# Optimization experiments

Measured on AMD Instinct MI355X. Metric: run time of the kernel, lower is better.

## Reference

```python
import math
import jax, jax.numpy as jnp
import numpy as np

B, N, C = 2, 2048, 4096
NUM_HEADS, KV_HEADS, HEAD_DIM = 32, 8, 128
N_REP = NUM_HEADS // KV_HEADS  # num_key_value_groups
MAX_SEQ = 4096


def rotate_half(x):
    h = x.shape[-1] // 2
    return jnp.concatenate([-x[..., h:], x[..., :h]], axis=-1)


def setup_inputs() -> dict:
    key = jax.random.key(0)
    k1, k2 = jax.random.split(key)
    inp = jax.random.normal(k1, (B, N, C), jnp.float32)
    sz = NUM_HEADS * HEAD_DIM + 2 * KV_HEADS * HEAD_DIM  # 6144
    weight = jax.random.normal(k2, (sz, C), jnp.float32) * 0.02
    # real LLaMA rotary caches [1,1,MAX_SEQ,HEAD_DIM]
    inv_freq = 1.0 / (10000.0 ** (jnp.arange(0, HEAD_DIM, 2, dtype=jnp.float32) / HEAD_DIM))
    t = jnp.arange(MAX_SEQ, dtype=jnp.float32)
    freqs = jnp.outer(t, inv_freq)
    emb = jnp.concatenate([freqs, freqs], axis=-1)
    cos_cached = jnp.cos(emb)[None, None]
    sin_cached = jnp.sin(emb)[None, None]
    neg = jnp.finfo(jnp.float32).min
    causal = jnp.where(jnp.tril(jnp.ones((N, N), dtype=bool)), 0.0, neg)
    attention_mask = jnp.broadcast_to(causal[None, None], (B, 1, N, N))
    position_ids = jnp.broadcast_to(jnp.arange(N, dtype=jnp.int32), (B, N))
    observation_mask = jnp.ones((B, N), dtype=jnp.int32)
    return dict(input=inp, weight=weight, cos_cached=cos_cached, sin_cached=sin_cached,
                attention_mask=attention_mask, position_ids=position_ids,
                observation_mask=observation_mask)


def reference(input, weight, cos_cached, sin_cached, attention_mask, position_ids, observation_mask):
    b, n, c = input.shape
    dtype = input.dtype
    qkv = input @ weight.T  # [B,N,6144]
    sz_q = NUM_HEADS * HEAD_DIM
    sz_kv = KV_HEADS * HEAD_DIM
    q = qkv[:, :, :sz_q].reshape(b, n, NUM_HEADS, HEAD_DIM).transpose(0, 2, 1, 3)
    k = qkv[:, :, sz_q:sz_q + sz_kv].reshape(b, n, KV_HEADS, HEAD_DIM).transpose(0, 2, 1, 3)
    v = qkv[:, :, sz_q + sz_kv:].reshape(b, n, KV_HEADS, HEAD_DIM).transpose(0, 2, 1, 3)
    # inline RoPE (HF llama apply_rotary_pos_emb)
    cos = cos_cached[0, 0][position_ids][:, None]  # [B,1,N,D]
    sin = sin_cached[0, 0][position_ids][:, None]
    q = q * cos + rotate_half(q) * sin
    k = k * cos + rotate_half(k) * sin
    # repeat_kv: expand kv heads to match q heads (each kv head repeated contiguously)
    k = jnp.repeat(k, N_REP, axis=1)
    v = jnp.repeat(v, N_REP, axis=1)
    attn = jnp.einsum('bhqd,bhkd->bhqk', q / math.sqrt(HEAD_DIM), k)
    attn = attn + attention_mask
    attn = jnp.maximum(attn, jnp.finfo(dtype).min)
    attn = jax.nn.softmax(attn.astype(jnp.float32), axis=-1).astype(dtype)
    out = jnp.einsum('bhqk,bhkd->bqhd', attn, v).reshape(b, n, c)
    # output[observation_mask == 1]: with an all-ones mask this is the flat [B*N, C] output;
    # expressed jit-safely as a multiplicative select
    out = out.reshape(b * n, c) * (observation_mask.reshape(-1, 1) == 1)
    return out.astype(jnp.float32)
```

## Files before the change

kernel.cpp:

```cpp
#include <hip/hip_runtime.h>
#include <hip/hip_bf16.h>
#include <stdint.h>

typedef __attribute__((ext_vector_type(8))) short bf16x8;
typedef __attribute__((ext_vector_type(4))) float f32x4;
typedef __attribute__((ext_vector_type(16))) float f32x16;

#define NB 2
#define NSEQ 2048
#define CDIM 4096
#define NH 32
#define NKV 8
#define HD 128
#define QKV_COLS 6144

static __device__ __forceinline__ unsigned short f2bf(float f) {
    union { float f; unsigned int u; } v; v.f = f;
    unsigned int r = v.u + 0x7fff + ((v.u >> 16) & 1);
    return (unsigned short)(r >> 16);
}
static __device__ __forceinline__ float bf2f(unsigned short b) {
    union { unsigned int u; float f; } v; v.u = ((unsigned int)b) << 16;
    return v.f;
}

static __device__ __forceinline__ void glds16(const void* g, void* l) {
    __builtin_amdgcn_global_load_lds(
        (const __attribute__((address_space(1))) void*)g,
        (__attribute__((address_space(3))) void*)l, 16, 0, 0);
}

static __device__ __forceinline__ unsigned cvtpk(float a, float b) {
    unsigned r; asm("v_cvt_pk_bf16_f32 %0, %1, %2" : "=v"(r) : "v"(a), "v"(b));
    return r;
}

static __device__ __forceinline__ void pack_tile(const f32x16& p, int l, bf16x8& fa, bf16x8& fb) {
    unsigned a0 = cvtpk(p[0], p[1]),   b0 = cvtpk(p[4], p[5]);
    unsigned a1 = cvtpk(p[2], p[3]),   b1 = cvtpk(p[6], p[7]);
    unsigned a2 = cvtpk(p[8], p[9]),   b2 = cvtpk(p[12], p[13]);
    unsigned a3 = cvtpk(p[10], p[11]), b3 = cvtpk(p[14], p[15]);
    union U { unsigned u[4]; bf16x8 v; } ua, ub;
#if __has_builtin(__builtin_amdgcn_permlane32_swap)
    auto r0 = __builtin_amdgcn_permlane32_swap(a0, b0, false, false);
    auto r1 = __builtin_amdgcn_permlane32_swap(a1, b1, false, false);
    auto r2 = __builtin_amdgcn_permlane32_swap(a2, b2, false, false);
    auto r3 = __builtin_amdgcn_permlane32_swap(a3, b3, false, false);
    ua.u[0] = r0[0]; ua.u[1] = r1[0]; ua.u[2] = r0[1]; ua.u[3] = r1[1];
    ub.u[0] = r2[0]; ub.u[1] = r3[0]; ub.u[2] = r2[1]; ub.u[3] = r3[1];
#else
    unsigned a0t = __shfl_xor(a0, 32), b0t = __shfl_xor(b0, 32);
    unsigned a1t = __shfl_xor(a1, 32), b1t = __shfl_xor(b1, 32);
    unsigned a2t = __shfl_xor(a2, 32), b2t = __shfl_xor(b2, 32);
    unsigned a3t = __shfl_xor(a3, 32), b3t = __shfl_xor(b3, 32);
    bool lo = (l < 32);
    ua.u[0] = lo ? a0 : b0t; ua.u[1] = lo ? a1 : b1t; ua.u[2] = lo ? a0t : b0; ua.u[3] = lo ? a1t : b1;
    ub.u[0] = lo ? a2 : b2t; ub.u[1] = lo ? a3 : b3t; ub.u[2] = lo ? a2t : b2; ub.u[3] = lo ? a3t : b3;
#endif
    fa = ua.v; fb = ub.v;
}

__global__ void convert_kernel(const float* __restrict__ inA, const float* __restrict__ inW,
                               unsigned short* __restrict__ outA, unsigned short* __restrict__ outW) {
    const long long nA4 = (long long)CDIM * (NB * NSEQ) / 4;
    const long long nW4 = (long long)QKV_COLS * CDIM / 4;
    const long long total = nA4 + nW4;
    for (long long i = blockIdx.x * 256LL + threadIdx.x; i < total; i += (long long)gridDim.x * 256LL) {
        const float4* src; unsigned short* dst; long long j;
        if (i < nA4) { src = (const float4*)inA; dst = outA; j = i; }
        else         { src = (const float4*)inW; dst = outW; j = i - nA4; }
        float4 v = src[j];
        ushort4 o;
        o.x = f2bf(v.x); o.y = f2bf(v.y); o.z = f2bf(v.z); o.w = f2bf(v.w);
        ((ushort4*)dst)[j] = o;
    }
}

#define GPHASE(PP, VNSTR, STAGES) do {                                                        \
    const int r0_ = wm*128 + (PP*2)*16 + lr16;                                                \
    const int r1_ = r0_ + 16;                                                                 \
    bf16x8 a00 = *(const bf16x8*)(lds + cur*32768 + r0_*128 + ((lc4*16) ^ ((r0_&7)<<4)));     \
    bf16x8 a01 = *(const bf16x8*)(lds + cur*32768 + r0_*128 + ((64+lc4*16) ^ ((r0_&7)<<4)));  \
    bf16x8 a10 = *(const bf16x8*)(lds + cur*32768 + r1_*128 + ((lc4*16) ^ ((r1_&7)<<4)));     \
    bf16x8 a11 = *(const bf16x8*)(lds + cur*32768 + r1_*128 + ((64+lc4*16) ^ ((r1_&7)<<4)));  \
    if (PP == 0) {                                                                            \
        _Pragma("unroll")                                                                     \
        for (int nf = 0; nf < 3; ++nf) {                                                      \
            int rb = wn*48 + nf*16 + lr16;                                                    \
            bfr[nf][0] = *(const bf16x8*)(lds + 65536 + cur*24576 + rb*128 + ((lc4*16) ^ ((rb&7)<<4)));    \
            bfr[nf][1] = *(const bf16x8*)(lds + 65536 + cur*24576 + rb*128 + ((64+lc4*16) ^ ((rb&7)<<4))); \
        }                                                                                     \
    }                                                                                         \
    STAGES;                                                                                   \
    __builtin_amdgcn_s_barrier();                                                             \
    asm volatile("s_waitcnt lgkmcnt(0)" ::: "memory");                                        \
    __builtin_amdgcn_s_setprio(1);                                                            \
    _Pragma("unroll")                                                                         \
    for (int nf = 0; nf < 3; ++nf) {                                                          \
        acc[PP*2  ][nf] = __builtin_amdgcn_mfma_f32_16x16x32_bf16(a00, bfr[nf][0], acc[PP*2  ][nf], 0,0,0); \
        acc[PP*2  ][nf] = __builtin_amdgcn_mfma_f32_16x16x32_bf16(a01, bfr[nf][1], acc[PP*2  ][nf], 0,0,0); \
        acc[PP*2+1][nf] = __builtin_amdgcn_mfma_f32_16x16x32_bf16(a10, bfr[nf][0], acc[PP*2+1][nf], 0,0,0); \
        acc[PP*2+1][nf] = __builtin_amdgcn_mfma_f32_16x16x32_bf16(a11, bfr[nf][1], acc[PP*2+1][nf], 0,0,0); \
    }                                                                                         \
    __builtin_amdgcn_s_setprio(0);                                                            \
    asm volatile("s_waitcnt " VNSTR ::: "memory");                                            \
    __builtin_amdgcn_s_barrier();                                                             \
} while (0)

__global__ __launch_bounds__(512) void gemm_qkv8(
    const unsigned short* __restrict__ A, const unsigned short* __restrict__ W,
    unsigned short* __restrict__ qb, unsigned short* __restrict__ kb, unsigned short* __restrict__ vt)
{
    __shared__ unsigned char lds[114688];
    const int bid0 = blockIdx.x;
    const int swz = (bid0 & 7) * 64 + (bid0 >> 3);
    const int bm = swz >> 5, bn = swz & 31;
    const int tid = threadIdx.x, l = tid & 63, w = tid >> 6;
    const int wm = w >> 2, wn = w & 3;
    const int lr16 = l & 15, lc4 = l >> 4;
    const int tid16 = tid * 16;
    const int abase = (tid >> 8) * 16384 + (tid & 255) * 16;

    f32x4 acc[8][3] = {};
    bf16x8 bfr[3][2];

    auto stageA = [&](int tb, int kt, int d) {
        int r = d >> 7, c = d & 127;
        int cs = c ^ ((r & 7) << 4);
        glds16(A + (long long)(bm * 256 + r) * CDIM + kt * 64 + (cs >> 1), lds + tb * 32768 + d);
    };
    auto stageB = [&](int tb, int kt, int d) {
        int r = d >> 7, c = d & 127;
        int cs = c ^ ((r & 7) << 4);
        glds16(W + (long long)(bn * 192 + r) * CDIM + kt * 64 + (cs >> 1), lds + 65536 + tb * 24576 + d);
    };

    stageB(0, 0, tid16); stageB(0, 0, tid16 + 8192); stageB(0, 0, tid16 + 16384);
    stageA(0, 0, abase); stageA(0, 0, abase + 4096); stageA(0, 0, abase + 8192); stageA(0, 0, abase + 12288);
    asm volatile("s_waitcnt vmcnt(0)" ::: "memory");
    __builtin_amdgcn_s_barrier();

    for (int t = 0; t < 64; ++t) {
        const int cur = t & 1, tb = cur ^ 1;
        const int tn = (t + 1 < 64) ? t + 1 : 63;
        GPHASE(0, "vmcnt(4)", { stageB(tb, tn, tid16);         stageB(tb, tn, tid16 + 8192); });
        GPHASE(1, "vmcnt(5)", { stageB(tb, tn, tid16 + 16384); stageA(tb, tn, abase);        });
        GPHASE(2, "vmcnt(6)", { stageA(tb, tn, abase + 4096);  stageA(tb, tn, abase + 8192); });
        GPHASE(3, "vmcnt(3)", { stageA(tb, tn, abase + 12288); });
    }

#pragma unroll
    for (int mf = 0; mf < 8; ++mf) {
        int gm0 = bm * 256 + wm * 128 + mf * 16 + lc4 * 4;
        int b = gm0 >> 11, n0 = gm0 & 2047;
#pragma unroll
        for (int nf = 0; nf < 3; ++nf) {
            int coln = bn * 192 + wn * 48 + nf * 16 + lr16;
            if (coln < 4096) {
                unsigned short* dst = qb + (((long long)(b * NH + (coln >> 7)) * NSEQ + n0) << 7) + (coln & 127);
#pragma unroll
                for (int r = 0; r < 4; ++r) dst[(long long)r << 7] = f2bf(acc[mf][nf][r]);
            } else if (coln < 5120) {
                int ck = coln - 4096;
                unsigned short* dst = kb + (((long long)(b * NKV + (ck >> 7)) * NSEQ + n0) << 7) + (ck & 127);
#pragma unroll
                for (int r = 0; r < 4; ++r) dst[(long long)r << 7] = f2bf(acc[mf][nf][r]);
            } else {
                int cv = coln - 5120;
                ushort4 o4;
                o4.x = f2bf(acc[mf][nf][0]); o4.y = f2bf(acc[mf][nf][1]);
                o4.z = f2bf(acc[mf][nf][2]); o4.w = f2bf(acc[mf][nf][3]);
                *(ushort4*)(vt + (((long long)(b * NKV + (cv >> 7)) * HD + (cv & 127)) << 11) + n0) = o4;
            }
        }
    }
}

__global__ void rope_kernel(unsigned short* __restrict__ qb, unsigned short* __restrict__ kb,
                            const float* __restrict__ cosc, const float* __restrict__ sinc,
                            const int* __restrict__ pos) {
    int rowid = blockIdx.x * 4 + (threadIdx.x >> 6);
    int d = threadIdx.x & 63;
    int b = rowid / (40 * NSEQ);
    int rem = rowid % (40 * NSEQ);
    int head = rem / NSEQ, n = rem % NSEQ;
    unsigned short* p;
    float scale;
    if (head < NH) { p = qb + (((long long)(b * NH + head) * NSEQ + n) << 7); scale = 0.12751747934f; }
    else           { p = kb + (((long long)(b * NKV + (head - NH)) * NSEQ + n) << 7); scale = 1.0f; }
    int pid = pos[b * NSEQ + n];
    float c = cosc[pid * HD + d], s = sinc[pid * HD + d];
    float x0 = bf2f(p[d]), x1 = bf2f(p[d + 64]);
    p[d]      = f2bf((x0 * c - x1 * s) * scale);
    p[d + 64] = f2bf((x1 * c + x0 * s) * scale);
}

__global__ __launch_bounds__(512) void attn_kernel(
    const unsigned short* __restrict__ qb, const unsigned short* __restrict__ kb,
    const unsigned short* __restrict__ vt, const int* __restrict__ obs,
    float* __restrict__ out)
{
    __shared__ unsigned char k_tile[2][16384];
    __shared__ unsigned char v_tile[2][16384];

    const int bid = blockIdx.x;
    const int qt = 7 - (bid >> 6);
    const int bh = bid & 63;
    const int b = bh >> 5, h = bh & 31, kvh = h >> 2;
    const int t = threadIdx.x, l = t & 63, w = t >> 6;
    const int lr = l & 31, hi = l >> 5;
    const int swl = (l & 7) << 4;

    const unsigned short* Qb = qb + (((long long)(b * NH + h) * NSEQ + qt * 256 + w * 32) << 7);
    const unsigned short* Kb = kb + (((long long)(b * NKV + kvh) * NSEQ) << 7);
    const unsigned short* Vb = vt + (((long long)(b * NKV + kvh) * HD) << 11);

    bf16x8 qf[8];
#pragma unroll
    for (int dk = 0; dk < 8; ++dk)
        qf[dk] = *(const bf16x8*)(Qb + lr * 128 + dk * 16 + hi * 8);

    f32x16 o[4];
#pragma unroll
    for (int dt = 0; dt < 4; ++dt)
#pragma unroll
        for (int e = 0; e < 16; ++e) o[dt][e] = 0.f;
    float m_run = -1e30f, l_run = 0.f;

    const int qwmax = qt * 256 + w * 32 + 31;
    const int niter = 4 * qt + 4;

    auto stage = [&](int kt, int tb) {
#pragma unroll
        for (int i = 0; i < 2; ++i) {
            int byte = (i * 512 + t) * 16;
            { int r = byte >> 8, c = byte & 255; int cs = c ^ ((r & 7) << 4);
              glds16(Kb + (((long long)(kt * 64 + r)) << 7) + (cs >> 1), k_tile[tb] + byte); }
            { int r = byte >> 7, c = byte & 127; int cs = c ^ ((r & 7) << 4);
              glds16(Vb + (((long long)r) << 11) + kt * 64 + (cs >> 1), v_tile[tb] + byte); }
        }
    };

    stage(0, 0);
    asm volatile("s_waitcnt vmcnt(0)" ::: "memory");
    __syncthreads();

    for (int kt = 0; kt < niter; ++kt) {
        const int cur = kt & 1;
        if (kt + 1 < niter) stage(kt + 1, cur ^ 1);

        if (kt * 64 <= qwmax) {
            f32x16 s0, s1;
#pragma unroll
            for (int e = 0; e < 16; ++e) { s0[e] = 0.f; s1[e] = 0.f; }
            __builtin_amdgcn_s_setprio(1);
#pragma unroll
            for (int dk = 0; dk < 8; ++dk) {
                int cb = (dk * 32 + hi * 16) ^ swl;
                bf16x8 k0 = *(const bf16x8*)(k_tile[cur] + lr * 256 + cb);
                bf16x8 k1 = *(const bf16x8*)(k_tile[cur] + (32 + lr) * 256 + cb);
                s0 = __builtin_amdgcn_mfma_f32_32x32x16_bf16(k0, qf[dk], s0, 0, 0, 0);
                s1 = __builtin_amdgcn_mfma_f32_32x32x16_bf16(k1, qf[dk], s1, 0, 0, 0);
            }
            __builtin_amdgcn_s_setprio(0);

            if (kt * 64 + 63 > qt * 256 + w * 32) {
                int qg = qt * 256 + w * 32 + lr;
                int base = kt * 64 + hi * 4;
#pragma unroll
                for (int e = 0; e < 16; ++e) {
                    int kv0 = base + (e & 3) + 8 * (e >> 2);
                    if (kv0 > qg)      s0[e] = -1e30f;
                    if (kv0 + 32 > qg) s1[e] = -1e30f;
                }
            }

            float mloc = fmaxf(s0[0], s0[1]);
#pragma unroll
            for (int e = 2; e < 16; ++e) mloc = fmaxf(mloc, s0[e]);
#pragma unroll
            for (int e = 0; e < 16; ++e) mloc = fmaxf(mloc, s1[e]);
            mloc = fmaxf(mloc, __shfl_xor(mloc, 32));

            float mm = m_run;
            if (!__all(mloc - m_run <= 8.f)) {
                mm = fmaxf(m_run, mloc);
                float sc = __builtin_amdgcn_exp2f(m_run - mm);
                l_run *= sc;
#pragma unroll
                for (int dt = 0; dt < 4; ++dt)
#pragma unroll
                    for (int e = 0; e < 16; ++e) o[dt][e] *= sc;
                m_run = mm;
            }
            float sum = 0.f;
#pragma unroll
            for (int e = 0; e < 16; ++e) { s0[e] = __builtin_amdgcn_exp2f(s0[e] - mm); sum += s0[e]; }
#pragma unroll
            for (int e = 0; e < 16; ++e) { s1[e] = __builtin_amdgcn_exp2f(s1[e] - mm); sum += s1[e]; }
            sum += __shfl_xor(sum, 32);
            l_run += sum;

            bf16x8 pb[4];
            pack_tile(s0, l, pb[0], pb[1]);
            pack_tile(s1, l, pb[2], pb[3]);

            __builtin_amdgcn_s_setprio(1);
#pragma unroll
            for (int dt = 0; dt < 4; ++dt) {
#pragma unroll
                for (int kk = 0; kk < 4; ++kk) {
                    int cb = (kk * 32 + hi * 16) ^ swl;
                    bf16x8 vf = *(const bf16x8*)(v_tile[cur] + (dt * 32 + lr) * 128 + cb);
                    o[dt] = __builtin_amdgcn_mfma_f32_32x32x16_bf16(vf, pb[kk], o[dt], 0, 0, 0);
                }
            }
            __builtin_amdgcn_s_setprio(0);
        }

        asm volatile("s_waitcnt vmcnt(0)" ::: "memory");
        __syncthreads();
    }

    {
        int n = qt * 256 + w * 32 + lr;
        float fac = (1.f / l_run) * ((obs[b * NSEQ + n] == 1) ? 1.f : 0.f);
        unsigned char* slice = &k_tile[0][0] + w * 4096;
        int q2 = l >> 1, half = l & 1;
        long long orow = ((long long)(b * NSEQ + qt * 256 + w * 32 + q2)) << 12;
#pragma unroll
        for (int dt = 0; dt < 4; ++dt) {
#pragma unroll
            for (int e = 0; e < 16; e += 2) {
                int dl = (e & 3) + 8 * (e >> 2) + hi * 4;
                int byte = (lr * 128 + dl * 4) ^ ((lr & 7) << 4);
                *(float2*)(slice + byte) = make_float2(o[dt][e] * fac, o[dt][e + 1] * fac);
            }
#pragma unroll
            for (int j = 0; j < 4; ++j) {
                int byte = (q2 * 128 + half * 64 + j * 16) ^ ((q2 & 7) << 4);
                f32x4 vv = *(const f32x4*)(slice + byte);
                *(f32x4*)(out + orow + h * 128 + dt * 32 + half * 16 + j * 4) = vv;
            }
            __syncthreads();
        }
    }
}

extern "C" void kernel_launch(void* const* d_in, const int* in_sizes, int n_in,
                              void* d_out, int out_size, void* d_ws, size_t ws_size,
                              hipStream_t stream) {
    (void)in_sizes; (void)n_in; (void)out_size; (void)ws_size;
    const float* inp  = (const float*)d_in[0];
    const float* wgt  = (const float*)d_in[1];
    const float* cosc = (const float*)d_in[2];
    const float* sinc = (const float*)d_in[3];
    const int* pos = (const int*)d_in[5];
    const int* obs = (const int*)d_in[6];
    float* out = (float*)d_out;

    char* ws = (char*)d_ws;
    unsigned short* A16 = (unsigned short*)(ws);
    unsigned short* W16 = (unsigned short*)(ws + 33554432LL);
    unsigned short* qb  = (unsigned short*)(ws + 83886080LL);
    unsigned short* kb  = (unsigned short*)(ws + 117440512LL);
    unsigned short* vt  = (unsigned short*)(ws + 125829120LL);

    convert_kernel<<<2048, 256, 0, stream>>>(inp, wgt, A16, W16);
    gemm_qkv8<<<512, 512, 0, stream>>>(A16, W16, qb, kb, vt);
    rope_kernel<<<(2 * 40 * NSEQ) / 4, 256, 0, stream>>>(qb, kb, cosc, sinc, pos);
    attn_kernel<<<512, 512, 0, stream>>>(qb, kb, vt, obs, out);
}
```

Measured before the change: 348.0 us.

## Load QKV GEMM B fragments directly from global into registers, skipping LDS

The weight (B) operand of the QKV projection GEMM is no longer staged through shared memory. Each wave now loads its B fragments straight from global memory into double-buffered registers one k-step ahead, and only the A tile goes through LDS. This cuts LDS use from 112KB to 64KB, removes the B LDS writes and reads, and may allow more occupancy. In exchange, B global loads are no longer shared across the wm waves, so the same W rows are fetched twice per block, and the vmcnt wait counts had to be retuned.

Result: slower. 481.1 us (+38.2%).

```diff
diff --git a/kernel.cpp b/kernel.cpp
--- a/kernel.cpp
+++ b/kernel.cpp
@@ -76,77 +76,80 @@
     }
 }
 
-#define GPHASE(PP, VNSTR, STAGES) do {                                                        \
+#define GPH(PP, VNSTR, BCUR, STG) do {                                                        \
     const int r0_ = wm*128 + (PP*2)*16 + lr16;                                                \
     const int r1_ = r0_ + 16;                                                                 \
     bf16x8 a00 = *(const bf16x8*)(lds + cur*32768 + r0_*128 + ((lc4*16) ^ ((r0_&7)<<4)));     \
     bf16x8 a01 = *(const bf16x8*)(lds + cur*32768 + r0_*128 + ((64+lc4*16) ^ ((r0_&7)<<4)));  \
     bf16x8 a10 = *(const bf16x8*)(lds + cur*32768 + r1_*128 + ((lc4*16) ^ ((r1_&7)<<4)));     \
     bf16x8 a11 = *(const bf16x8*)(lds + cur*32768 + r1_*128 + ((64+lc4*16) ^ ((r1_&7)<<4)));  \
-    if (PP == 0) {                                                                            \
-        _Pragma("unroll")                                                                     \
-        for (int nf = 0; nf < 3; ++nf) {                                                      \
-            int rb = wn*48 + nf*16 + lr16;                                                    \
-            bfr[nf][0] = *(const bf16x8*)(lds + 65536 + cur*24576 + rb*128 + ((lc4*16) ^ ((rb&7)<<4)));    \
-            bfr[nf][1] = *(const bf16x8*)(lds + 65536 + cur*24576 + rb*128 + ((64+lc4*16) ^ ((rb&7)<<4))); \
-        }                                                                                     \
-    }                                                                                         \
-    STAGES;                                                                                   \
+    STG;                                                                                      \
     __builtin_amdgcn_s_barrier();                                                             \
     asm volatile("s_waitcnt lgkmcnt(0)" ::: "memory");                                        \
     __builtin_amdgcn_s_setprio(1);                                                            \
     _Pragma("unroll")                                                                         \
     for (int nf = 0; nf < 3; ++nf) {                                                          \
-        acc[PP*2  ][nf] = __builtin_amdgcn_mfma_f32_16x16x32_bf16(a00, bfr[nf][0], acc[PP*2  ][nf], 0,0,0); \
-        acc[PP*2  ][nf] = __builtin_amdgcn_mfma_f32_16x16x32_bf16(a01, bfr[nf][1], acc[PP*2  ][nf], 0,0,0); \
-        acc[PP*2+1][nf] = __builtin_amdgcn_mfma_f32_16x16x32_bf16(a10, bfr[nf][0], acc[PP*2+1][nf], 0,0,0); \
-        acc[PP*2+1][nf] = __builtin_amdgcn_mfma_f32_16x16x32_bf16(a11, bfr[nf][1], acc[PP*2+1][nf], 0,0,0); \
+        acc[PP*2  ][nf] = __builtin_amdgcn_mfma_f32_16x16x32_bf16(a00, BCUR[nf][0], acc[PP*2  ][nf], 0,0,0); \
+        acc[PP*2  ][nf] = __builtin_amdgcn_mfma_f32_16x16x32_bf16(a01, BCUR[nf][1], acc[PP*2  ][nf], 0,0,0); \
+        acc[PP*2+1][nf] = __builtin_amdgcn_mfma_f32_16x16x32_bf16(a10, BCUR[nf][0], acc[PP*2+1][nf], 0,0,0); \
+        acc[PP*2+1][nf] = __builtin_amdgcn_mfma_f32_16x16x32_bf16(a11, BCUR[nf][1], acc[PP*2+1][nf], 0,0,0); \
     }                                                                                         \
     __builtin_amdgcn_s_setprio(0);                                                            \
     asm volatile("s_waitcnt " VNSTR ::: "memory");                                            \
     __builtin_amdgcn_s_barrier();                                                             \
 } while (0)
 
+#define GITER(T, BCUR, BNXT) do {                                                             \
+    const int cur = (T) & 1, tb = cur ^ 1;                                                    \
+    const int tn = ((T) + 1 < 64) ? (T) + 1 : 63;                                             \
+    GPH(0, "vmcnt(12)", BCUR, {                                                               \
+        _Pragma("unroll")                                                                     \
+        for (int nf2 = 0; nf2 < 3; ++nf2) {                                                   \
+            BNXT[nf2][0] = *(const bf16x8*)(Wrow + nf2 * 16 * CDIM + tn * 64);                \
+            BNXT[nf2][1] = *(const bf16x8*)(Wrow + nf2 * 16 * CDIM + tn * 64 + 32);           \
+        }                                                                                     \
+        stageA(tb, tn, abase);          stageA(tb, tn, abase + 4096);                         \
+        stageA(tb, tn, abase + 8192);   stageA(tb, tn, abase + 12288); });                    \
+    GPH(1, "vmcnt(11)", BCUR, {});                                                            \
+    GPH(2, "vmcnt(10)", BCUR, {});                                                            \
+    GPH(3, "vmcnt(2)",  BCUR, {});                                                            \
+} while (0)
+
 __global__ __launch_bounds__(512) void gemm_qkv8(
     const unsigned short* __restrict__ A, const unsigned short* __restrict__ W,
     unsigned short* __restrict__ qb, unsigned short* __restrict__ kb, unsigned short* __restrict__ vt)
 {
-    __shared__ unsigned char lds[114688];
+    __shared__ unsigned char lds[65536];
     const int bid0 = blockIdx.x;
     const int swz = (bid0 & 7) * 64 + (bid0 >> 3);
     const int bm = swz >> 5, bn = swz & 31;
     const int tid = threadIdx.x, l = tid & 63, w = tid >> 6;
     const int wm = w >> 2, wn = w & 3;
     const int lr16 = l & 15, lc4 = l >> 4;
-    const int tid16 = tid * 16;
     const int abase = (tid >> 8) * 16384 + (tid & 255) * 16;
 
     f32x4 acc[8][3] = {};
-    bf16x8 bfr[3][2];
+    bf16x8 bfrA[3][2], bfrB[3][2];
+    const unsigned short* Wrow = W + (long long)(bn * 192 + wn * 48 + lr16) * CDIM + lc4 * 8;
 
     auto stageA = [&](int tb, int kt, int d) {
         int r = d >> 7, c = d & 127;
         int cs = c ^ ((r & 7) << 4);
         glds16(A + (long long)(bm * 256 + r) * CDIM + kt * 64 + (cs >> 1), lds + tb * 32768 + d);
     };
-    auto stageB = [&](int tb, int kt, int d) {
-        int r = d >> 7, c = d & 127;
-        int cs = c ^ ((r & 7) << 4);
-        glds16(W + (long long)(bn * 192 + r) * CDIM + kt * 64 + (cs >> 1), lds + 65536 + tb * 24576 + d);
-    };
-
-    stageB(0, 0, tid16); stageB(0, 0, tid16 + 8192); stageB(0, 0, tid16 + 16384);
+
     stageA(0, 0, abase); stageA(0, 0, abase + 4096); stageA(0, 0, abase + 8192); stageA(0, 0, abase + 12288);
+#pragma unroll
+    for (int nf2 = 0; nf2 < 3; ++nf2) {
+        bfrA[nf2][0] = *(const bf16x8*)(Wrow + nf2 * 16 * CDIM);
+        bfrA[nf2][1] = *(const bf16x8*)(Wrow + nf2 * 16 * CDIM + 32);
+    }
     asm volatile("s_waitcnt vmcnt(0)" ::: "memory");
     __builtin_amdgcn_s_barrier();
 
-    for (int t = 0; t < 64; ++t) {
-        const int cur = t & 1, tb = cur ^ 1;
-        const int tn = (t + 1 < 64) ? t + 1 : 63;
-        GPHASE(0, "vmcnt(4)", { stageB(tb, tn, tid16);         stageB(tb, tn, tid16 + 8192); });
-        GPHASE(1, "vmcnt(5)", { stageB(tb, tn, tid16 + 16384); stageA(tb, tn, abase);        });
-        GPHASE(2, "vmcnt(6)", { stageA(tb, tn, abase + 4096);  stageA(tb, tn, abase + 8192); });
-        GPHASE(3, "vmcnt(3)", { stageA(tb, tn, abase + 12288); });
+    for (int t2 = 0; t2 < 64; t2 += 2) {
+        GITER(t2,     bfrA, bfrB);
+        GITER(t2 + 1, bfrB, bfrA);
     }
 
 #pragma unroll
```
